# Performance work log

Measured on AMD Instinct MI355X. Metric: run time of the kernel, lower is better.

Reference implementation:

```python
import jax, jax.numpy as jnp
import numpy as np

QTZ_BETA = 0.25


def setup_inputs() -> dict:
    key = jax.random.key(0)
    k1, k2 = jax.random.split(key)
    z = jax.random.normal(k1, (65536, 1, 256), dtype=jnp.float32)
    codebook = jax.random.normal(k2, (4096, 256), dtype=jnp.float32)
    return {"z": z, "codebook": codebook}


def reference(z, codebook):
    """Hard VQ quantization: nearest-codebook lookup with straight-through
    estimator plus codebook commitment loss. Returns (z_q, codebook_loss,
    min_embed_ids)."""
    D = codebook.shape[-1]
    z_f = z.reshape(-1, D)  # [N, D]
    # Pairwise squared L2 distances via expansion: ||z||^2 - 2 z c^T + ||c||^2
    # (argmin is invariant to the monotone transform vs. torch.cdist's sqrt)
    d2 = (
        jnp.sum(z_f * z_f, axis=1, keepdims=True)  # [N, 1]
        - 2.0 * (z_f @ codebook.T)                 # [N, K]
        + jnp.sum(codebook * codebook, axis=1)     # [K]
    )
    min_embed_ids = jnp.argmin(d2, axis=1)  # [N]
    # one_hot @ codebook is exactly a gather of codebook rows
    z_q = jnp.take(codebook, min_embed_ids, axis=0).reshape(z.shape)
    # Straight-through estimator
    z_q = z + jax.lax.stop_gradient(z_q - z)
    # Codebook loss (uses the STE z_q, matching the torch code)
    codebook_loss = (
        jnp.mean((jax.lax.stop_gradient(z_q) - z) ** 2)
        + jnp.mean((z_q - jax.lax.stop_gradient(z)) ** 2) * QTZ_BETA
    )
    return (z_q, codebook_loss, min_embed_ids)
```

## Files before the change

kernel.cpp:

```cpp
#include <hip/hip_runtime.h>
#include <stdint.h>

typedef _Float16 f16;
typedef _Float16 f16x4 __attribute__((ext_vector_type(4)));
typedef _Float16 f16x8 __attribute__((ext_vector_type(8)));
typedef float f32x4 __attribute__((ext_vector_type(4)));
typedef unsigned long long u64;

#define D_DIM 256
#define K_CB 4096
#define N_ROWS 65536
#define BM 128
#define BN 128
#define N_TILES 32
#define LOSS_OFF 16777216
#define IDS_OFF 16777217
#define MAX_FIX 4096

#define WS_CHI 0
#define WS_CN 2097152
#define WS_CNT 2113536
#define WS_ROWS 2113600
#define WS_SLOTS 2129984

#define GL_LDS(g, s_) __builtin_amdgcn_global_load_lds( \
    (const __attribute__((address_space(1))) void*)(g), \
    (__attribute__((address_space(3))) void*)(s_), 16, 0, 0)

static __device__ __forceinline__ uint32_t f2u(float x) { union { float f; uint32_t u; } c; c.f = x; return c.u; }
static __device__ __forceinline__ float u2f(uint32_t x) { union { float f; uint32_t u; } c; c.u = x; return c.f; }
static __device__ __forceinline__ uint32_t umin_(uint32_t a, uint32_t b) { return a < b ? a : b; }
static __device__ __forceinline__ uint32_t umax_(uint32_t a, uint32_t b) { return a > b ? a : b; }
static __device__ __forceinline__ u64 d2u(double x) { union { double d; u64 u; } c; c.d = x; return c.u; }

__global__ __launch_bounds__(256) void k_prep_cb(const float* __restrict__ cb,
                                                 f16* __restrict__ chi,
                                                 float* __restrict__ cn,
                                                 uint32_t* __restrict__ cnt,
                                                 u64* __restrict__ slots,
                                                 float* __restrict__ loss_slot) {
    const int tid = threadIdx.x;
    const int w = tid >> 6, l = tid & 63;
    const int row = blockIdx.x * 4 + w;
    const float4 v = ((const float4*)cb)[row * 64 + l];
    f16x4 h4;
    h4[0] = (f16)v.x; h4[1] = (f16)v.y; h4[2] = (f16)v.z; h4[3] = (f16)v.w;
    float ss = v.x * v.x + v.y * v.y + v.z * v.z + v.w * v.w;
#pragma unroll
    for (int m = 32; m >= 1; m >>= 1) ss += __shfl_xor(ss, m);
    ((f16x4*)chi)[row * 64 + l] = h4;
    if (l == 0) cn[row] = ss;
    if (tid < 4) slots[blockIdx.x * 4 + tid] = 0xFFFFFFFFFFFFFFFFull;
    if (blockIdx.x == 0 && tid == 0) { *cnt = 0; *loss_slot = 0.0f; }
}

__global__ __launch_bounds__(256) void k_main(const float* __restrict__ z,
                                              const float* __restrict__ cb,
                                              const f16* __restrict__ chi,
                                              const float* __restrict__ cn,
                                              uint32_t* __restrict__ cnt,
                                              uint32_t* __restrict__ rows,
                                              float* __restrict__ out) {
    extern __shared__ char smem[];
    const int tid = threadIdx.x;
    const int w = tid >> 6, l = tid & 63;
    const int wm = w >> 1, wn = w & 1;
    const int l15 = l & 15, qh = l >> 4;
    const int blk = blockIdx.x;
    const float* ztile = z + (size_t)blk * (BM * D_DIM);

#pragma unroll 4
    for (int p = 0; p < 32; ++p) {
        const int r = p * 4 + w;
        const float4 v = ((const float4*)ztile)[r * 64 + l];
        f16x4 h4;
        h4[0] = (f16)(v.x * -2.0f); h4[1] = (f16)(v.y * -2.0f);
        h4[2] = (f16)(v.z * -2.0f); h4[3] = (f16)(v.w * -2.0f);
        const int addr = r * 512 + ((((l >> 1) ^ (r & 7))) << 4) + ((l & 1) << 3);
        *(f16x4*)(smem + addr) = h4;
    }

    float cnNext[4];
#pragma unroll
    for (int j = 0; j < 4; ++j) cnNext[j] = cn[wn * 64 + j * 16 + l15];

    const int e0 = tid >> 2;
    const int q0 = (tid & 3) ^ ((e0 >> 1) & 3);
    const int offE = e0 * 256 + q0 * 8;

    int rowb[4], rs[4], bcon[4];
#pragma unroll
    for (int i = 0; i < 4; ++i) {
        const int r = wm * 64 + i * 16 + l15;
        rowb[i] = r * 512;
        rs[i] = r & 7;
    }
#pragma unroll
    for (int j = 0; j < 4; ++j) {
        const int e = wn * 64 + j * 16 + l15;
        bcon[j] = e * 64 + ((qh ^ ((e >> 1) & 3)) << 4);
    }

    {
        const f16* gh = chi + offE;
        char* bb = smem + 65536 + w * 1024;
        GL_LDS(gh, bb);
        GL_LDS(gh + 16384, bb + 4096);
    }

    uint32_t k1[16], k2[16], k3[16];
#pragma unroll
    for (int s = 0; s < 16; ++s) { k1[s] = 0xFFFFFFFFu; k2[s] = 0xFFFFFFFFu; k3[s] = 0xFFFFFFFFu; }
    f32x4 acc[4][4];
    float cnCur[4];

    for (int tile = 0; tile < N_TILES; ++tile) {
#pragma unroll
        for (int j = 0; j < 4; ++j) cnCur[j] = cnNext[j];
#pragma unroll
        for (int j = 0; j < 4; ++j) {
            const float base = cnCur[j] + 64.0f;
#pragma unroll
            for (int i = 0; i < 4; ++i) acc[i][j] = (f32x4){base, base, base, base};
        }
#pragma unroll
        for (int kc = 0; kc < 8; ++kc) {
            __syncthreads();
            const int step = tile * 8 + kc;
            if (step + 1 < N_TILES * 8) {
                const int nt = (step + 1) >> 3, nk = (step + 1) & 7;
                const f16* gh = chi + nt * (BN * D_DIM) + nk * 32 + offE;
                char* bb = smem + 65536 + ((step + 1) & 1) * 8192 + w * 1024;
                GL_LDS(gh, bb);
                GL_LDS(gh + 16384, bb + 4096);
            }
            if (kc == 0) {
                const int tn = (tile + 1 < N_TILES) ? tile + 1 : tile;
#pragma unroll
                for (int j = 0; j < 4; ++j)
                    cnNext[j] = cn[tn * BN + wn * 64 + j * 16 + l15];
            }
            const char* bbase = smem + 65536 + (step & 1) * 8192;
            f16x8 ah[4], bh[4];
#pragma unroll
            for (int i = 0; i < 4; ++i) {
                const int t = ((kc << 2) + qh) ^ rs[i];
                ah[i] = *(const f16x8*)(smem + rowb[i] + (t << 4));
            }
#pragma unroll
            for (int j = 0; j < 4; ++j) bh[j] = *(const f16x8*)(bbase + bcon[j]);
#pragma unroll
            for (int i = 0; i < 4; ++i)
#pragma unroll
                for (int j = 0; j < 4; ++j)
                    acc[i][j] = __builtin_amdgcn_mfma_f32_16x16x32_f16(ah[i], bh[j], acc[i][j], 0, 0, 0);
        }
        const int colb = tile * BN + wn * 64 + l15;
#pragma unroll
        for (int j = 0; j < 4; ++j) {
            const uint32_t col = (uint32_t)(colb + j * 16);
#pragma unroll
            for (int i = 0; i < 4; ++i)
#pragma unroll
                for (int rr = 0; rr < 4; ++rr) {
                    const int s = i * 4 + rr;
                    const uint32_t kk = (f2u(acc[i][j][rr]) & 0xFFFFF000u) | col;
                    const uint32_t t2 = umax_(k1[s], kk); k1[s] = umin_(k1[s], kk);
                    const uint32_t t3 = umax_(k2[s], t2); k2[s] = umin_(k2[s], t2);
                    k3[s] = umin_(k3[s], t3);
                }
        }
    }

#pragma unroll
    for (int s = 0; s < 16; ++s) {
        uint32_t a1 = k1[s], a2 = k2[s], a3 = k3[s];
#pragma unroll
        for (int m = 1; m <= 8; m <<= 1) {
            const uint32_t b1 = (uint32_t)__shfl_xor((int)a1, m);
            const uint32_t b2 = (uint32_t)__shfl_xor((int)a2, m);
            const uint32_t b3 = (uint32_t)__shfl_xor((int)a3, m);
            const uint32_t x = umax_(a1, b1);
            const uint32_t m2v = umin_(a2, b2), M2 = umax_(a2, b2);
            const uint32_t m3v = umin_(a3, b3);
            a1 = umin_(a1, b1);
            a2 = umin_(x, m2v);
            a3 = umin_(umin_(umax_(x, m2v), M2), m3v);
        }
        k1[s] = a1; k2[s] = a2; k3[s] = a3;
    }
    __syncthreads();
    uint32_t* mk = (uint32_t*)(smem + 65536);
    double* lossW = (double*)(smem + 65536 + 1536);
    if (wn == 0 && l15 == 0) {
#pragma unroll
        for (int s = 0; s < 16; ++s) {
            const int row = wm * 64 + (s >> 2) * 16 + qh * 4 + (s & 3);
            mk[row] = k1[s]; mk[128 + row] = k2[s]; mk[256 + row] = k3[s];
        }
    }
    __syncthreads();
    if (wn == 1 && l15 == 0) {
#pragma unroll
        for (int s = 0; s < 16; ++s) {
            const int row = wm * 64 + (s >> 2) * 16 + qh * 4 + (s & 3);
            const uint32_t b1 = mk[row], b2 = mk[128 + row], b3 = mk[256 + row];
            const uint32_t x = umax_(k1[s], b1);
            const uint32_t m2v = umin_(k2[s], b2), M2 = umax_(k2[s], b2);
            const uint32_t m3v = umin_(k3[s], b3);
            mk[row] = umin_(k1[s], b1);
            mk[128 + row] = umin_(x, m2v);
            mk[256 + row] = umin_(umin_(umax_(x, m2v), M2), m3v);
        }
    }
    __syncthreads();

    double lossAcc = 0.0;
    for (int it = 0; it < 32; ++it) {
        const int row = it * 4 + w;
        const uint32_t K1 = mk[row], K2 = mk[128 + row], K3 = mk[256 + row];
        const int col1 = (int)(K1 & 4095u), col2 = (int)(K2 & 4095u);
        const float4 c1 = ((const float4*)cb)[col1 * 64 + l];
        const float4 c2 = ((const float4*)cb)[col2 * 64 + l];
        const float4 z4 = ((const float4*)ztile)[row * 64 + l];
        double e1, e2;
        {
            const double dx1 = (double)c1.x - z4.x, dy1 = (double)c1.y - z4.y;
            const double dz1 = (double)c1.z - z4.z, dw1 = (double)c1.w - z4.w;
            e1 = dx1 * dx1 + dy1 * dy1 + dz1 * dz1 + dw1 * dw1;
            const double dx2 = (double)c2.x - z4.x, dy2 = (double)c2.y - z4.y;
            const double dz2 = (double)c2.z - z4.z, dw2 = (double)c2.w - z4.w;
            e2 = dx2 * dx2 + dy2 * dy2 + dz2 * dz2 + dw2 * dw2;
        }
        float zn2 = z4.x * z4.x + z4.y * z4.y + z4.z * z4.z + z4.w * z4.w;
#pragma unroll
        for (int m = 32; m >= 1; m >>= 1) {
            e1 += __shfl_xor(e1, m);
            e2 += __shfl_xor(e2, m);
            zn2 += __shfl_xor(zn2, m);
        }
        const bool take1 = (e1 < e2) || (e1 == e2 && col1 <= col2);
        const float4 cw = take1 ? c1 : c2;
        ((float4*)out)[(blk * BM + row) * 64 + l] = cw;
        if (l == 0) {
            const int colw = take1 ? col1 : col2;
            const double ew = take1 ? e1 : e2;
            out[IDS_OFF + blk * BM + row] = (float)colw;
            lossAcc += ew;
            const float d3 = u2f(K3 & 0xFFFFF000u) + zn2 - 64.0f;
            const float eps = 0.006f * sqrtf(zn2) + 0.01f;
            if (!((float)ew < d3 - eps)) {
                const uint32_t e = atomicAdd(cnt, 1u);
                if (e < MAX_FIX) rows[e] = (uint32_t)(blk * BM + row);
            }
        }
    }
    if (l == 0) lossW[w] = lossAcc;
    __syncthreads();
    if (tid == 0) {
        const double tot = (lossW[0] + lossW[1] + lossW[2] + lossW[3]) * (1.25 / 16777216.0);
        atomicAdd(out + LOSS_OFF, (float)tot);
    }
}

__global__ __launch_bounds__(256) void k_fix_scan(const float* __restrict__ z,
                                                  const float* __restrict__ cb,
                                                  const uint32_t* __restrict__ cnt,
                                                  const uint32_t* __restrict__ rows,
                                                  u64* __restrict__ slots) {
    __shared__ float zrow[256];
    __shared__ u64 wmin[4];
    const int tid = threadIdx.x;
    const int w = tid >> 6, l = tid & 63;
    const int chunk = blockIdx.x & 15;
    uint32_t n = *cnt; if (n > MAX_FIX) n = MAX_FIX;
    for (uint32_t e = blockIdx.x >> 4; e < n; e += 64) {
        const int row = (int)rows[e];
        __syncthreads();
        if (tid < 64) ((float4*)zrow)[tid] = ((const float4*)z)[row * 64 + tid];
        __syncthreads();
        const int c = chunk * 256 + tid;
        const float4* crow = (const float4*)(cb + (size_t)c * 256);
        double s = 0.0;
        for (int q = 0; q < 64; ++q) {
            const float4 cv = crow[q];
            const float4 zv = ((const float4*)zrow)[q];
            const double dx = (double)cv.x - zv.x, dy = (double)cv.y - zv.y;
            const double dz = (double)cv.z - zv.z, dw = (double)cv.w - zv.w;
            s += dx * dx + dy * dy + dz * dz + dw * dw;
        }
        u64 key = (d2u(s) & 0xFFFFFFFFFFFFF000ull) | (u64)c;
#pragma unroll
        for (int m = 32; m >= 1; m >>= 1) {
            const u64 o = __shfl_xor(key, m);
            if (o < key) key = o;
        }
        if (l == 0) wmin[w] = key;
        __syncthreads();
        if (tid == 0) {
            u64 k = wmin[0];
            if (wmin[1] < k) k = wmin[1];
            if (wmin[2] < k) k = wmin[2];
            if (wmin[3] < k) k = wmin[3];
            atomicMin(&slots[e], k);
        }
    }
}

__global__ __launch_bounds__(256) void k_fix_patch(const float* __restrict__ z,
                                                   const float* __restrict__ cb,
                                                   const uint32_t* __restrict__ cnt,
                                                   const uint32_t* __restrict__ rows,
                                                   const u64* __restrict__ slots,
                                                   float* __restrict__ out) {
    const int tid = threadIdx.x;
    uint32_t n = *cnt; if (n > MAX_FIX) n = MAX_FIX;
    for (uint32_t e = blockIdx.x; e < n; e += 256) {
        const int row = (int)rows[e];
        const int newc = (int)(slots[e] & 4095ull);
        const int oldc = (int)out[IDS_OFF + row];
        if (newc == oldc) continue;
        double dOld = 0.0, dNew = 0.0;
        if (tid < 64) {
            const float4 zv = ((const float4*)z)[row * 64 + tid];
            const float4 co = ((const float4*)cb)[oldc * 64 + tid];
            const float4 cn4 = ((const float4*)cb)[newc * 64 + tid];
            const double ax = (double)co.x - zv.x, ay = (double)co.y - zv.y;
            const double az = (double)co.z - zv.z, aw = (double)co.w - zv.w;
            dOld = ax * ax + ay * ay + az * az + aw * aw;
            const double bx = (double)cn4.x - zv.x, by = (double)cn4.y - zv.y;
            const double bz = (double)cn4.z - zv.z, bw = (double)cn4.w - zv.w;
            dNew = bx * bx + by * by + bz * bz + bw * bw;
            ((float4*)out)[row * 64 + tid] = cn4;
        }
#pragma unroll
        for (int m = 32; m >= 1; m >>= 1) {
            dOld += __shfl_xor(dOld, m);
            dNew += __shfl_xor(dNew, m);
        }
        if (tid == 0) {
            out[IDS_OFF + row] = (float)newc;
            atomicAdd(out + LOSS_OFF, (float)((dNew - dOld) * (1.25 / 16777216.0)));
        }
    }
}

extern "C" void kernel_launch(void* const* d_in, const int* in_sizes, int n_in,
                              void* d_out, int out_size, void* d_ws, size_t ws_size,
                              hipStream_t stream) {
    (void)in_sizes; (void)n_in; (void)out_size; (void)ws_size;
    const float* z = (const float*)d_in[0];
    const float* cb = (const float*)d_in[1];
    float* out = (float*)d_out;
    char* ws = (char*)d_ws;
    f16* chi = (f16*)(ws + WS_CHI);
    float* cn = (float*)(ws + WS_CN);
    uint32_t* cnt = (uint32_t*)(ws + WS_CNT);
    uint32_t* rows = (uint32_t*)(ws + WS_ROWS);
    u64* slots = (u64*)(ws + WS_SLOTS);

    hipFuncSetAttribute((const void*)k_main,
                        hipFuncAttributeMaxDynamicSharedMemorySize, 81920);

    k_prep_cb<<<K_CB / 4, 256, 0, stream>>>(cb, chi, cn, cnt, slots, out + LOSS_OFF);
    k_main<<<N_ROWS / BM, 256, 81920, stream>>>(z, cb, chi, cn, cnt, rows, out);
    k_fix_scan<<<1024, 256, 0, stream>>>(z, cb, cnt, rows, slots);
    k_fix_patch<<<256, 256, 0, stream>>>(z, cb, cnt, rows, slots, out);
}
```

Before: 307.1 us.

## Double-buffer accumulators to overlap top-3 selection with next tile's MFMAs

The tile loop now runs in pairs with two accumulator sets. The top-3 insertion for the previous tile is spread across the 8 k-steps of the current tile, so the VALU selection work interleaves with MFMA issue instead of running as a serial epilogue. Insertion and merge use v_med3_u32 and v_min3_u32 to cut instruction count, and the launch bounds now request 2 waves per SIMD. Keeping a second 64-register accumulator set raises register pressure and may cause spills under the new occupancy bound.

```diff
diff --git a/kernel.cpp b/kernel.cpp
--- a/kernel.cpp
+++ b/kernel.cpp
@@ -32,6 +32,25 @@
 static __device__ __forceinline__ uint32_t umin_(uint32_t a, uint32_t b) { return a < b ? a : b; }
 static __device__ __forceinline__ uint32_t umax_(uint32_t a, uint32_t b) { return a > b ? a : b; }
 static __device__ __forceinline__ u64 d2u(double x) { union { double d; u64 u; } c; c.d = x; return c.u; }
+
+static __device__ __forceinline__ uint32_t med3u(uint32_t a, uint32_t b, uint32_t c) {
+    uint32_t d;
+    asm("v_med3_u32 %0, %1, %2, %3" : "=v"(d) : "v"(a), "v"(b), "v"(c));
+    return d;
+}
+static __device__ __forceinline__ uint32_t min3u(uint32_t a, uint32_t b, uint32_t c) {
+    uint32_t d;
+    asm("v_min3_u32 %0, %1, %2, %3" : "=v"(d) : "v"(a), "v"(b), "v"(c));
+    return d;
+}
+
+#define INS3(s_, kk_) do { \
+    const uint32_t kkv_ = (kk_); \
+    const uint32_t n1_ = umin_(k1[s_], kkv_); \
+    const uint32_t n2_ = med3u(kkv_, k1[s_], k2[s_]); \
+    const uint32_t n3_ = med3u(kkv_, k2[s_], k3[s_]); \
+    k1[s_] = n1_; k2[s_] = n2_; k3[s_] = n3_; \
+} while (0)
 
 __global__ __launch_bounds__(256) void k_prep_cb(const float* __restrict__ cb,
                                                  f16* __restrict__ chi,
@@ -54,13 +73,62 @@
     if (blockIdx.x == 0 && tid == 0) { *cnt = 0; *loss_slot = 0.0f; }
 }
 
-__global__ __launch_bounds__(256) void k_main(const float* __restrict__ z,
-                                              const float* __restrict__ cb,
-                                              const f16* __restrict__ chi,
-                                              const float* __restrict__ cn,
-                                              uint32_t* __restrict__ cnt,
-                                              uint32_t* __restrict__ rows,
-                                              float* __restrict__ out) {
+#define TILE_BODY(ACC, PREV, TILE) do { \
+    const int tile_ = (TILE); \
+    _Pragma("unroll") for (int j = 0; j < 4; ++j) cnCur[j] = cnNext[j]; \
+    _Pragma("unroll") for (int j = 0; j < 4; ++j) { \
+        const float base_ = cnCur[j] + 64.0f; \
+        _Pragma("unroll") for (int i = 0; i < 4; ++i) \
+            ACC[i][j] = (f32x4){base_, base_, base_, base_}; \
+    } \
+    const int prevColb_ = (tile_ - 1) * BN + wn * 64 + l15; \
+    _Pragma("unroll") for (int kc = 0; kc < 8; ++kc) { \
+        __syncthreads(); \
+        const int step_ = tile_ * 8 + kc; \
+        if (step_ + 1 < N_TILES * 8) { \
+            const int nt_ = (step_ + 1) >> 3, nk_ = (step_ + 1) & 7; \
+            const f16* gh_ = chi + nt_ * (BN * D_DIM) + nk_ * 32 + offE; \
+            char* bb_ = smem + 65536 + ((kc + 1) & 1) * 8192 + w * 1024; \
+            GL_LDS(gh_, bb_); \
+            GL_LDS(gh_ + 16384, bb_ + 4096); \
+        } \
+        if (kc == 0) { \
+            const int tn_ = (tile_ + 1 < N_TILES) ? tile_ + 1 : tile_; \
+            _Pragma("unroll") for (int j = 0; j < 4; ++j) \
+                cnNext[j] = cn[tn_ * BN + wn * 64 + j * 16 + l15]; \
+        } \
+        const char* bbase_ = smem + 65536 + (kc & 1) * 8192; \
+        f16x8 ah[4], bh[4]; \
+        _Pragma("unroll") for (int i = 0; i < 4; ++i) { \
+            const int t_ = ((kc << 2) + qh) ^ rs[i]; \
+            ah[i] = *(const f16x8*)(smem + rowb[i] + (t_ << 4)); \
+        } \
+        _Pragma("unroll") for (int j = 0; j < 4; ++j) \
+            bh[j] = *(const f16x8*)(bbase_ + bcon[j]); \
+        {  \
+            const int pi_ = kc >> 1; \
+            _Pragma("unroll") for (int jj = 0; jj < 2; ++jj) { \
+                const int pj_ = (kc & 1) * 2 + jj; \
+                const uint32_t col_ = (uint32_t)(prevColb_ + pj_ * 16); \
+                _Pragma("unroll") for (int rr = 0; rr < 4; ++rr) { \
+                    const uint32_t kk_ = (f2u(PREV[pi_][pj_][rr]) & 0xFFFFF000u) | col_; \
+                    INS3(pi_ * 4 + rr, kk_); \
+                } \
+            } \
+        } \
+        _Pragma("unroll") for (int i = 0; i < 4; ++i) \
+            _Pragma("unroll") for (int j = 0; j < 4; ++j) \
+                ACC[i][j] = __builtin_amdgcn_mfma_f32_16x16x32_f16(ah[i], bh[j], ACC[i][j], 0, 0, 0); \
+    } \
+} while (0)
+
+__global__ __launch_bounds__(256, 2) void k_main(const float* __restrict__ z,
+                                                 const float* __restrict__ cb,
+                                                 const f16* __restrict__ chi,
+                                                 const float* __restrict__ cn,
+                                                 uint32_t* __restrict__ cnt,
+                                                 uint32_t* __restrict__ rows,
+                                                 float* __restrict__ out) {
     extern __shared__ char smem[];
     const int tid = threadIdx.x;
     const int w = tid >> 6, l = tid & 63;
@@ -111,51 +179,23 @@
     uint32_t k1[16], k2[16], k3[16];
 #pragma unroll
     for (int s = 0; s < 16; ++s) { k1[s] = 0xFFFFFFFFu; k2[s] = 0xFFFFFFFFu; k3[s] = 0xFFFFFFFFu; }
-    f32x4 acc[4][4];
+
+    f32x4 accA[4][4], accB[4][4];
+    {
+        const float iv = __builtin_inff();
+#pragma unroll
+        for (int i = 0; i < 4; ++i)
+#pragma unroll
+            for (int j = 0; j < 4; ++j) accB[i][j] = (f32x4){iv, iv, iv, iv};
+    }
     float cnCur[4];
 
-    for (int tile = 0; tile < N_TILES; ++tile) {
-#pragma unroll
-        for (int j = 0; j < 4; ++j) cnCur[j] = cnNext[j];
-#pragma unroll
-        for (int j = 0; j < 4; ++j) {
-            const float base = cnCur[j] + 64.0f;
-#pragma unroll
-            for (int i = 0; i < 4; ++i) acc[i][j] = (f32x4){base, base, base, base};
-        }
-#pragma unroll
-        for (int kc = 0; kc < 8; ++kc) {
-            __syncthreads();
-            const int step = tile * 8 + kc;
-            if (step + 1 < N_TILES * 8) {
-                const int nt = (step + 1) >> 3, nk = (step + 1) & 7;
-                const f16* gh = chi + nt * (BN * D_DIM) + nk * 32 + offE;
-                char* bb = smem + 65536 + ((step + 1) & 1) * 8192 + w * 1024;
-                GL_LDS(gh, bb);
-                GL_LDS(gh + 16384, bb + 4096);
-            }
-            if (kc == 0) {
-                const int tn = (tile + 1 < N_TILES) ? tile + 1 : tile;
-#pragma unroll
-                for (int j = 0; j < 4; ++j)
-                    cnNext[j] = cn[tn * BN + wn * 64 + j * 16 + l15];
-            }
-            const char* bbase = smem + 65536 + (step & 1) * 8192;
-            f16x8 ah[4], bh[4];
-#pragma unroll
-            for (int i = 0; i < 4; ++i) {
-                const int t = ((kc << 2) + qh) ^ rs[i];
-                ah[i] = *(const f16x8*)(smem + rowb[i] + (t << 4));
-            }
-#pragma unroll
-            for (int j = 0; j < 4; ++j) bh[j] = *(const f16x8*)(bbase + bcon[j]);
-#pragma unroll
-            for (int i = 0; i < 4; ++i)
-#pragma unroll
-                for (int j = 0; j < 4; ++j)
-                    acc[i][j] = __builtin_amdgcn_mfma_f32_16x16x32_f16(ah[i], bh[j], acc[i][j], 0, 0, 0);
-        }
-        const int colb = tile * BN + wn * 64 + l15;
+    for (int tp = 0; tp < N_TILES; tp += 2) {
+        TILE_BODY(accA, accB, tp);
+        TILE_BODY(accB, accA, tp + 1);
+    }
+    {
+        const int colb = (N_TILES - 1) * BN + wn * 64 + l15;
 #pragma unroll
         for (int j = 0; j < 4; ++j) {
             const uint32_t col = (uint32_t)(colb + j * 16);
@@ -163,11 +203,8 @@
             for (int i = 0; i < 4; ++i)
 #pragma unroll
                 for (int rr = 0; rr < 4; ++rr) {
-                    const int s = i * 4 + rr;
-                    const uint32_t kk = (f2u(acc[i][j][rr]) & 0xFFFFF000u) | col;
-                    const uint32_t t2 = umax_(k1[s], kk); k1[s] = umin_(k1[s], kk);
-                    const uint32_t t3 = umax_(k2[s], t2); k2[s] = umin_(k2[s], t2);
-                    k3[s] = umin_(k3[s], t3);
+                    const uint32_t kk = (f2u(accB[i][j][rr]) & 0xFFFFF000u) | col;
+                    INS3(i * 4 + rr, kk);
                 }
         }
     }
@@ -180,12 +217,10 @@
             const uint32_t b1 = (uint32_t)__shfl_xor((int)a1, m);
             const uint32_t b2 = (uint32_t)__shfl_xor((int)a2, m);
             const uint32_t b3 = (uint32_t)__shfl_xor((int)a3, m);
-            const uint32_t x = umax_(a1, b1);
-            const uint32_t m2v = umin_(a2, b2), M2 = umax_(a2, b2);
-            const uint32_t m3v = umin_(a3, b3);
-            a1 = umin_(a1, b1);
-            a2 = umin_(x, m2v);
-            a3 = umin_(umin_(umax_(x, m2v), M2), m3v);
+            const uint32_t r1 = umin_(a1, b1);
+            const uint32_t r2 = min3u(a2, b2, umax_(a1, b1));
+            const uint32_t r3 = min3u(umax_(a1, b2), umax_(a2, b1), umin_(a3, b3));
+            a1 = r1; a2 = r2; a3 = r3;
         }
         k1[s] = a1; k2[s] = a2; k3[s] = a3;
     }
@@ -205,12 +240,9 @@
         for (int s = 0; s < 16; ++s) {
             const int row = wm * 64 + (s >> 2) * 16 + qh * 4 + (s & 3);
             const uint32_t b1 = mk[row], b2 = mk[128 + row], b3 = mk[256 + row];
-            const uint32_t x = umax_(k1[s], b1);
-            const uint32_t m2v = umin_(k2[s], b2), M2 = umax_(k2[s], b2);
-            const uint32_t m3v = umin_(k3[s], b3);
             mk[row] = umin_(k1[s], b1);
-            mk[128 + row] = umin_(x, m2v);
-            mk[256 + row] = umin_(umin_(umax_(x, m2v), M2), m3v);
+            mk[128 + row] = min3u(k2[s], b2, umax_(k1[s], b1));
+            mk[256 + row] = min3u(umax_(k1[s], b2), umax_(k2[s], b1), umin_(k3[s], b3));
         }
     }
     __syncthreads();
```

Result: faster. 295.8 us (-3.7%).

## Split main VQ kernel across 8 waves with kc-major A layout and med3 top-3

Applied to the files above, without the earlier changes.

Doubles the main kernel's block to 512 threads so each wave covers 32 rows instead of 64, halving accumulators and top-3 state per thread. The A tile moves to a kc-major swizzled LDS layout, and each thread now issues one codebook LDS load per step instead of two. The per-step __syncthreads is replaced by an explicit vmcnt wait plus s_barrier. Top-3 insertion and merging use v_med3/v_min3 to cut VALU ops. The goal is more latency hiding and fewer epilogue instructions, at the cost of more barrier participants per block and possibly lower occupancy from LDS use.

```diff
diff --git a/kernel.cpp b/kernel.cpp
--- a/kernel.cpp
+++ b/kernel.cpp
@@ -23,6 +23,8 @@
 #define WS_ROWS 2113600
 #define WS_SLOTS 2129984
 
+#define LDS_BYTES 81920
+
 #define GL_LDS(g, s_) __builtin_amdgcn_global_load_lds( \
     (const __attribute__((address_space(1))) void*)(g), \
     (__attribute__((address_space(3))) void*)(s_), 16, 0, 0)
@@ -32,6 +34,25 @@
 static __device__ __forceinline__ uint32_t umin_(uint32_t a, uint32_t b) { return a < b ? a : b; }
 static __device__ __forceinline__ uint32_t umax_(uint32_t a, uint32_t b) { return a > b ? a : b; }
 static __device__ __forceinline__ u64 d2u(double x) { union { double d; u64 u; } c; c.d = x; return c.u; }
+
+static __device__ __forceinline__ uint32_t med3u(uint32_t a, uint32_t b, uint32_t c) {
+    uint32_t d;
+    asm("v_med3_u32 %0, %1, %2, %3" : "=v"(d) : "v"(a), "v"(b), "v"(c));
+    return d;
+}
+static __device__ __forceinline__ uint32_t min3u(uint32_t a, uint32_t b, uint32_t c) {
+    uint32_t d;
+    asm("v_min3_u32 %0, %1, %2, %3" : "=v"(d) : "v"(a), "v"(b), "v"(c));
+    return d;
+}
+
+#define INS3(s_, kk_) do { \
+    const uint32_t kkv_ = (kk_); \
+    const uint32_t n1_ = umin_(k1[s_], kkv_); \
+    const uint32_t n2_ = med3u(kkv_, k1[s_], k2[s_]); \
+    const uint32_t n3_ = med3u(kkv_, k2[s_], k3[s_]); \
+    k1[s_] = n1_; k2[s_] = n2_; k3[s_] = n3_; \
+} while (0)
 
 __global__ __launch_bounds__(256) void k_prep_cb(const float* __restrict__ cb,
                                                  f16* __restrict__ chi,
@@ -54,13 +75,13 @@
     if (blockIdx.x == 0 && tid == 0) { *cnt = 0; *loss_slot = 0.0f; }
 }
 
-__global__ __launch_bounds__(256) void k_main(const float* __restrict__ z,
-                                              const float* __restrict__ cb,
-                                              const f16* __restrict__ chi,
-                                              const float* __restrict__ cn,
-                                              uint32_t* __restrict__ cnt,
-                                              uint32_t* __restrict__ rows,
-                                              float* __restrict__ out) {
+__global__ __launch_bounds__(512, 4) void k_main(const float* __restrict__ z,
+                                                 const float* __restrict__ cb,
+                                                 const f16* __restrict__ chi,
+                                                 const float* __restrict__ cn,
+                                                 uint32_t* __restrict__ cnt,
+                                                 uint32_t* __restrict__ rows,
+                                                 float* __restrict__ out) {
     extern __shared__ char smem[];
     const int tid = threadIdx.x;
     const int w = tid >> 6, l = tid & 63;
@@ -69,14 +90,25 @@
     const int blk = blockIdx.x;
     const float* ztile = z + (size_t)blk * (BM * D_DIM);
 
+    const int e0 = tid >> 2;
+    const int q0 = (tid & 3) ^ ((e0 >> 1) & 3);
+    const int offE = e0 * 256 + q0 * 8;
+
+    {
+        const f16* gh = chi + offE;
+        char* bb = smem + 65536 + w * 1024;
+        GL_LDS(gh, bb);
+    }
+
 #pragma unroll 4
-    for (int p = 0; p < 32; ++p) {
-        const int r = p * 4 + w;
+    for (int p = 0; p < 16; ++p) {
+        const int r = p * 8 + w;
         const float4 v = ((const float4*)ztile)[r * 64 + l];
         f16x4 h4;
         h4[0] = (f16)(v.x * -2.0f); h4[1] = (f16)(v.y * -2.0f);
         h4[2] = (f16)(v.z * -2.0f); h4[3] = (f16)(v.w * -2.0f);
-        const int addr = r * 512 + ((((l >> 1) ^ (r & 7))) << 4) + ((l & 1) << 3);
+        const int kcw = l >> 3, q = (l >> 1) & 3, half = l & 1;
+        const int addr = kcw * 8192 + r * 64 + (((q ^ ((r >> 1) & 3))) << 4) + half * 8;
         *(f16x4*)(smem + addr) = h4;
     }
 
@@ -84,55 +116,41 @@
 #pragma unroll
     for (int j = 0; j < 4; ++j) cnNext[j] = cn[wn * 64 + j * 16 + l15];
 
-    const int e0 = tid >> 2;
-    const int q0 = (tid & 3) ^ ((e0 >> 1) & 3);
-    const int offE = e0 * 256 + q0 * 8;
-
-    int rowb[4], rs[4], bcon[4];
-#pragma unroll
-    for (int i = 0; i < 4; ++i) {
-        const int r = wm * 64 + i * 16 + l15;
-        rowb[i] = r * 512;
-        rs[i] = r & 7;
-    }
+    const int ab = wm * 2048 + l15 * 64 + ((qh ^ ((l15 >> 1) & 3)) << 4);
+
+    int bcon[4];
 #pragma unroll
     for (int j = 0; j < 4; ++j) {
         const int e = wn * 64 + j * 16 + l15;
         bcon[j] = e * 64 + ((qh ^ ((e >> 1) & 3)) << 4);
     }
 
-    {
-        const f16* gh = chi + offE;
-        char* bb = smem + 65536 + w * 1024;
-        GL_LDS(gh, bb);
-        GL_LDS(gh + 16384, bb + 4096);
-    }
-
-    uint32_t k1[16], k2[16], k3[16];
-#pragma unroll
-    for (int s = 0; s < 16; ++s) { k1[s] = 0xFFFFFFFFu; k2[s] = 0xFFFFFFFFu; k3[s] = 0xFFFFFFFFu; }
-    f32x4 acc[4][4];
-    float cnCur[4];
+    uint32_t k1[8], k2[8], k3[8];
+#pragma unroll
+    for (int s = 0; s < 8; ++s) { k1[s] = 0xFFFFFFFFu; k2[s] = 0xFFFFFFFFu; k3[s] = 0xFFFFFFFFu; }
+
+    f32x4 acc[2][4];
+
+    __syncthreads();
 
     for (int tile = 0; tile < N_TILES; ++tile) {
 #pragma unroll
-        for (int j = 0; j < 4; ++j) cnCur[j] = cnNext[j];
-#pragma unroll
         for (int j = 0; j < 4; ++j) {
-            const float base = cnCur[j] + 64.0f;
-#pragma unroll
-            for (int i = 0; i < 4; ++i) acc[i][j] = (f32x4){base, base, base, base};
+            const float base = cnNext[j] + 64.0f;
+#pragma unroll
+            for (int i = 0; i < 2; ++i) acc[i][j] = (f32x4){base, base, base, base};
         }
 #pragma unroll
         for (int kc = 0; kc < 8; ++kc) {
-            __syncthreads();
             const int step = tile * 8 + kc;
+            asm volatile("s_waitcnt vmcnt(0)" ::: "memory");
+            __builtin_amdgcn_s_barrier();
+            __builtin_amdgcn_sched_barrier(0);
             if (step + 1 < N_TILES * 8) {
                 const int nt = (step + 1) >> 3, nk = (step + 1) & 7;
                 const f16* gh = chi + nt * (BN * D_DIM) + nk * 32 + offE;
-                char* bb = smem + 65536 + ((step + 1) & 1) * 8192 + w * 1024;
+                char* bb = smem + 65536 + ((kc + 1) & 1) * 8192 + w * 1024;
                 GL_LDS(gh, bb);
-                GL_LDS(gh + 16384, bb + 4096);
             }
             if (kc == 0) {
                 const int tn = (tile + 1 < N_TILES) ? tile + 1 : tile;
@@ -140,17 +158,15 @@
                 for (int j = 0; j < 4; ++j)
                     cnNext[j] = cn[tn * BN + wn * 64 + j * 16 + l15];
             }
-            const char* bbase = smem + 65536 + (step & 1) * 8192;
-            f16x8 ah[4], bh[4];
-#pragma unroll
-            for (int i = 0; i < 4; ++i) {
-                const int t = ((kc << 2) + qh) ^ rs[i];
-                ah[i] = *(const f16x8*)(smem + rowb[i] + (t << 4));
-            }
+            const char* bbase = smem + 65536 + (kc & 1) * 8192;
+            f16x8 ah[2], bh[4];
+#pragma unroll
+            for (int i = 0; i < 2; ++i)
+                ah[i] = *(const f16x8*)(smem + ab + kc * 8192 + i * 1024);
 #pragma unroll
             for (int j = 0; j < 4; ++j) bh[j] = *(const f16x8*)(bbase + bcon[j]);
 #pragma unroll
-            for (int i = 0; i < 4; ++i)
+            for (int i = 0; i < 2; ++i)
 #pragma unroll
                 for (int j = 0; j < 4; ++j)
                     acc[i][j] = __builtin_amdgcn_mfma_f32_16x16x32_f16(ah[i], bh[j], acc[i][j], 0, 0, 0);
@@ -160,32 +176,27 @@
         for (int j = 0; j < 4; ++j) {
             const uint32_t col = (uint32_t)(colb + j * 16);
 #pragma unroll
-            for (int i = 0; i < 4; ++i)
+            for (int i = 0; i < 2; ++i)
 #pragma unroll
                 for (int rr = 0; rr < 4; ++rr) {
-                    const int s = i * 4 + rr;
                     const uint32_t kk = (f2u(acc[i][j][rr]) & 0xFFFFF000u) | col;
-                    const uint32_t t2 = umax_(k1[s], kk); k1[s] = umin_(k1[s], kk);
-                    const uint32_t t3 = umax_(k2[s], t2); k2[s] = umin_(k2[s], t2);
-                    k3[s] = umin_(k3[s], t3);
+                    INS3(i * 4 + rr, kk);
                 }
         }
     }
 
 #pragma unroll
-    for (int s = 0; s < 16; ++s) {
+    for (int s = 0; s < 8; ++s) {
         uint32_t a1 = k1[s], a2 = k2[s], a3 = k3[s];
 #pragma unroll
         for (int m = 1; m <= 8; m <<= 1) {
             const uint32_t b1 = (uint32_t)__shfl_xor((int)a1, m);
             const uint32_t b2 = (uint32_t)__shfl_xor((int)a2, m);
             const uint32_t b3 = (uint32_t)__shfl_xor((int)a3, m);
-            const uint32_t x = umax_(a1, b1);
-            const uint32_t m2v = umin_(a2, b2), M2 = umax_(a2, b2);
-            const uint32_t m3v = umin_(a3, b3);
-            a1 = umin_(a1, b1);
-            a2 = umin_(x, m2v);
-            a3 = umin_(umin_(umax_(x, m2v), M2), m3v);
+            const uint32_t r1 = umin_(a1, b1);
+            const uint32_t r2 = min3u(a2, b2, umax_(a1, b1));
+            const uint32_t r3 = min3u(umax_(a1, b2), umax_(a2, b1), umin_(a3, b3));
+            a1 = r1; a2 = r2; a3 = r3;
         }
         k1[s] = a1; k2[s] = a2; k3[s] = a3;
     }
@@ -194,30 +205,27 @@
     double* lossW = (double*)(smem + 65536 + 1536);
     if (wn == 0 && l15 == 0) {
 #pragma unroll
-        for (int s = 0; s < 16; ++s) {
-            const int row = wm * 64 + (s >> 2) * 16 + qh * 4 + (s & 3);
+        for (int s = 0; s < 8; ++s) {
+            const int row = wm * 32 + (s >> 2) * 16 + qh * 4 + (s & 3);
             mk[row] = k1[s]; mk[128 + row] = k2[s]; mk[256 + row] = k3[s];
         }
     }
     __syncthreads();
     if (wn == 1 && l15 == 0) {
 #pragma unroll
-        for (int s = 0; s < 16; ++s) {
-            const int row = wm * 64 + (s >> 2) * 16 + qh * 4 + (s & 3);
+        for (int s = 0; s < 8; ++s) {
+            const int row = wm * 32 + (s >> 2) * 16 + qh * 4 + (s & 3);
             const uint32_t b1 = mk[row], b2 = mk[128 + row], b3 = mk[256 + row];
-            const uint32_t x = umax_(k1[s], b1);
-            const uint32_t m2v = umin_(k2[s], b2), M2 = umax_(k2[s], b2);
-            const uint32_t m3v = umin_(k3[s], b3);
             mk[row] = umin_(k1[s], b1);
-            mk[128 + row] = umin_(x, m2v);
-            mk[256 + row] = umin_(umin_(umax_(x, m2v), M2), m3v);
+            mk[128 + row] = min3u(k2[s], b2, umax_(k1[s], b1));
+            mk[256 + row] = min3u(umax_(k1[s], b2), umax_(k2[s], b1), umin_(k3[s], b3));
         }
     }
     __syncthreads();
 
     double lossAcc = 0.0;
-    for (int it = 0; it < 32; ++it) {
-        const int row = it * 4 + w;
+    for (int it = 0; it < 16; ++it) {
+        const int row = it * 8 + w;
         const uint32_t K1 = mk[row], K2 = mk[128 + row], K3 = mk[256 + row];
         const int col1 = (int)(K1 & 4095u), col2 = (int)(K2 & 4095u);
         const float4 c1 = ((const float4*)cb)[col1 * 64 + l];
@@ -258,8 +266,10 @@
     if (l == 0) lossW[w] = lossAcc;
     __syncthreads();
     if (tid == 0) {
-        const double tot = (lossW[0] + lossW[1] + lossW[2] + lossW[3]) * (1.25 / 16777216.0);
-        atomicAdd(out + LOSS_OFF, (float)tot);
+        double tot = 0.0;
+#pragma unroll
+        for (int i = 0; i < 8; ++i) tot += lossW[i];
+        atomicAdd(out + LOSS_OFF, (float)(tot * (1.25 / 16777216.0)));
     }
 }
 
@@ -360,10 +370,10 @@
     u64* slots = (u64*)(ws + WS_SLOTS);
 
     hipFuncSetAttribute((const void*)k_main,
-                        hipFuncAttributeMaxDynamicSharedMemorySize, 81920);
+                        hipFuncAttributeMaxDynamicSharedMemorySize, LDS_BYTES);
 
     k_prep_cb<<<K_CB / 4, 256, 0, stream>>>(cb, chi, cn, cnt, slots, out + LOSS_OFF);
-    k_main<<<N_ROWS / BM, 256, 81920, stream>>>(z, cb, chi, cn, cnt, rows, out);
+    k_main<<<N_ROWS / BM, 512, LDS_BYTES, stream>>>(z, cb, chi, cn, cnt, rows, out);
     k_fix_scan<<<1024, 256, 0, stream>>>(z, cb, cnt, rows, slots);
     k_fix_patch<<<256, 256, 0, stream>>>(z, cb, cnt, rows, slots, out);
 }
```

Result: faster. 290.2 us (-5.5%).
